# Optimization experiments

Measured on AMD Instinct MI355X. Metric: run time of the kernel, lower is better.

Reference implementation:

```python
import jax, jax.numpy as jnp
import numpy as np

TEMPERATURE = 12.5      # EMDLayer temperature
SINKHORN_EPS = 0.05     # entropic regularization for the batched EMD solve
SINKHORN_ITERS = 50     # fixed iteration count (jit-friendly)
WEIGHT_EPS = 1e-05      # OpenCVSolver adds 1e-5 after relu


def setup_inputs() -> dict:
    key = jax.random.key(0)
    k1, k2, k3 = jax.random.split(key, 3)
    E, Q, W, N = 4, 75, 5, 64
    similarity_map = jax.random.uniform(k1, (E, Q, W, N, N), dtype=jnp.float32)
    weight_1 = jax.random.uniform(k2, (E, Q, W, N), dtype=jnp.float32)
    weight_2 = jax.random.uniform(k3, (E, W, Q, N), dtype=jnp.float32)
    return {"similarity_map": similarity_map, "weight_1": weight_1, "weight_2": weight_2}


def _emd_flow(cost, a, b):
    """Batched entropic-regularized EMD (log-domain Sinkhorn).
    cost: [B, N, N]; a, b: [B, N] positive marginals (each sums to N).
    Returns flow: [B, N, N] with row sums ~a and col sums ~b."""
    logK = -cost / SINKHORN_EPS            # [B, N, N]
    log_a = jnp.log(a)
    log_b = jnp.log(b)

    def step(carry, _):
        log_u, log_v = carry
        log_u = log_a - jax.scipy.special.logsumexp(logK + log_v[:, None, :], axis=2)
        log_v = log_b - jax.scipy.special.logsumexp(logK + log_u[:, :, None], axis=1)
        return (log_u, log_v), None

    init = (jnp.zeros_like(log_a), jnp.zeros_like(log_b))
    (log_u, log_v), _ = jax.lax.scan(step, init, None, length=SINKHORN_ITERS)
    return jnp.exp(logK + log_u[:, :, None] + log_v[:, None, :])


def reference(similarity_map, weight_1, weight_2):
    E, Q, W, N, _ = similarity_map.shape
    sim = similarity_map.reshape(-1, N, N)                       # [B, N, N]
    w1 = weight_1.reshape(-1, N)                                  # [B, N]
    w2 = jnp.transpose(weight_2, (0, 2, 1, 3)).reshape(-1, N)     # transpose(1,2) then flatten

    # OpenCVSolver weight preprocessing: relu + eps, renormalize to sum N
    w1 = jax.nn.relu(w1) + WEIGHT_EPS
    w1 = w1 * (N / jnp.sum(w1, axis=1, keepdims=True))
    w2 = jax.nn.relu(w2) + WEIGHT_EPS
    w2 = w2 * (N / jnp.sum(w2, axis=1, keepdims=True))

    cost = 1.0 - sim
    flow = _emd_flow(cost, w1, w2)                                # [B, N, N]
    scores = jnp.sum(flow * sim, axis=(-1, -2)).reshape(E, Q, W)
    return scores * (TEMPERATURE / N)
```

## Files before the change

### kernel.cpp

```cpp
#include <hip/hip_runtime.h>

#define N 64
#define NPAD 65
#define ITERS 50
#define TEMP 12.5f
#define WEPS 1e-5f
#define QDIM 75
#define WDIM 5

__device__ __forceinline__ float waveReduceSum(float x) {
#pragma unroll
    for (int off = 32; off; off >>= 1) x += __shfl_xor(x, off, 64);
    return x;
}

__global__ __launch_bounds__(64) void emd_sinkhorn_kernel(
    const float* __restrict__ sim,
    const float* __restrict__ w1,
    const float* __restrict__ w2,
    float* __restrict__ out,
    int B)
{
    __shared__ __align__(16) float S[N * NPAD];
    __shared__ __align__(16) float U[N];
    __shared__ __align__(16) float V[N];

    const int b    = blockIdx.x;
    const int lane = threadIdx.x;
    const float* g = sim + (size_t)b * N * N;

    const float4* g4 = (const float4*)g;
#pragma unroll
    for (int t = 0; t < 16; ++t) {
        float4 x = g4[t * 64 + lane];
        int e0 = (t * 64 + lane) * 4;
        int r = e0 >> 6;
        int c = e0 & 63;
        S[r * NPAD + c + 0] = x.x;
        S[r * NPAD + c + 1] = x.y;
        S[r * NPAD + c + 2] = x.z;
        S[r * NPAD + c + 3] = x.w;
    }
    __syncthreads();

    float Krow[N], Kcol[N];
#pragma unroll
    for (int j = 0; j < N; ++j)
        Krow[j] = __expf((S[lane * NPAD + j] - 1.0f) * 20.0f);
#pragma unroll
    for (int i = 0; i < N; ++i)
        Kcol[i] = __expf((S[i * NPAD + lane] - 1.0f) * 20.0f);

    float a = w1[(size_t)b * N + lane];
    a = fmaxf(a, 0.0f) + WEPS;
    a *= (float)N / waveReduceSum(a);

    const int e   = b / (QDIM * WDIM);
    const int rem = b % (QDIM * WDIM);
    const int q   = rem / WDIM;
    const int w   = rem % WDIM;
    float bb = w2[((((size_t)e * WDIM + w) * QDIM) + q) * N + lane];
    bb = fmaxf(bb, 0.0f) + WEPS;
    bb *= (float)N / waveReduceSum(bb);

    V[lane] = 1.0f;
    __syncthreads();

    float u = 0.0f, v = 1.0f;
#pragma unroll 1
    for (int it = 0; it < ITERS; ++it) {
        const float4* V4 = (const float4*)V;
        float acc0 = 0, acc1 = 0, acc2 = 0, acc3 = 0;
#pragma unroll
        for (int j4 = 0; j4 < 16; ++j4) {
            float4 vv = V4[j4];
            acc0 = fmaf(Krow[4 * j4 + 0], vv.x, acc0);
            acc1 = fmaf(Krow[4 * j4 + 1], vv.y, acc1);
            acc2 = fmaf(Krow[4 * j4 + 2], vv.z, acc2);
            acc3 = fmaf(Krow[4 * j4 + 3], vv.w, acc3);
        }
        u = a * __builtin_amdgcn_rcpf((acc0 + acc1) + (acc2 + acc3));
        U[lane] = u;
        __syncthreads();

        const float4* U4 = (const float4*)U;
        acc0 = 0; acc1 = 0; acc2 = 0; acc3 = 0;
#pragma unroll
        for (int i4 = 0; i4 < 16; ++i4) {
            float4 uu = U4[i4];
            acc0 = fmaf(Kcol[4 * i4 + 0], uu.x, acc0);
            acc1 = fmaf(Kcol[4 * i4 + 1], uu.y, acc1);
            acc2 = fmaf(Kcol[4 * i4 + 2], uu.z, acc2);
            acc3 = fmaf(Kcol[4 * i4 + 3], uu.w, acc3);
        }
        v = bb * __builtin_amdgcn_rcpf((acc0 + acc1) + (acc2 + acc3));
        V[lane] = v;
        __syncthreads();
    }

    float s0 = 0, s1 = 0, s2 = 0, s3 = 0;
#pragma unroll
    for (int j4 = 0; j4 < 16; ++j4) {
        float4 vv = ((const float4*)V)[j4];
        s0 = fmaf(Krow[4 * j4 + 0] * S[lane * NPAD + 4 * j4 + 0], vv.x, s0);
        s1 = fmaf(Krow[4 * j4 + 1] * S[lane * NPAD + 4 * j4 + 1], vv.y, s1);
        s2 = fmaf(Krow[4 * j4 + 2] * S[lane * NPAD + 4 * j4 + 2], vv.z, s2);
        s3 = fmaf(Krow[4 * j4 + 3] * S[lane * NPAD + 4 * j4 + 3], vv.w, s3);
    }
    float partial = u * ((s0 + s1) + (s2 + s3));
    float tot = waveReduceSum(partial);
    if (lane == 0) out[b] = tot * (TEMP / (float)N);
}

extern "C" void kernel_launch(void* const* d_in, const int* in_sizes, int n_in,
                              void* d_out, int out_size, void* d_ws, size_t ws_size,
                              hipStream_t stream) {
    const float* sim = (const float*)d_in[0];
    const float* w1  = (const float*)d_in[1];
    const float* w2  = (const float*)d_in[2];
    float* out       = (float*)d_out;
    const int B = in_sizes[0] / (N * N);
    emd_sinkhorn_kernel<<<B, 64, 0, stream>>>(sim, w1, w2, out, B);
}
```

Measured before the change: 111.4 us.

## Split each Sinkhorn problem across four wavefronts with quad shuffle reductions

Each block now uses 256 threads instead of 64. Every row or column is handled by four lanes that each hold 16 kernel entries in registers and combine their partial dot products with xor shuffles. The per-thread register footprint drops from 128 kernel values to 32, and the serial dependent FMA chain per iteration gets shorter. In exchange, each half-iteration barrier now synchronises four wavefronts, and the redundant U/V shared-memory reads add LDS traffic.

```diff
diff --git a/kernel.cpp b/kernel.cpp
--- a/kernel.cpp
+++ b/kernel.cpp
@@ -14,102 +14,128 @@
     return x;
 }
 
-__global__ __launch_bounds__(64) void emd_sinkhorn_kernel(
+__global__ __launch_bounds__(256, 1) void emd_sinkhorn4w(
     const float* __restrict__ sim,
     const float* __restrict__ w1,
     const float* __restrict__ w2,
     float* __restrict__ out,
     int B)
 {
-    __shared__ __align__(16) float S[N * NPAD];
-    __shared__ __align__(16) float U[N];
-    __shared__ __align__(16) float V[N];
+    __shared__ float S[N * NPAD];
+    __shared__ __align__(16) float U[N], V[N], A[N], Bm[N];
+    __shared__ float Wred[4];
 
+    const int t    = threadIdx.x;
+    const int lane = t & 63;
+    const int wv   = t >> 6;
     const int b    = blockIdx.x;
-    const int lane = threadIdx.x;
-    const float* g = sim + (size_t)b * N * N;
+    const int r    = t >> 2;
+    const int j4   = t & 3;
+    const int c0   = j4 * 16;
 
-    const float4* g4 = (const float4*)g;
+    const float4* g4 = (const float4*)(sim + (size_t)b * N * N);
 #pragma unroll
-    for (int t = 0; t < 16; ++t) {
-        float4 x = g4[t * 64 + lane];
-        int e0 = (t * 64 + lane) * 4;
-        int r = e0 >> 6;
-        int c = e0 & 63;
-        S[r * NPAD + c + 0] = x.x;
-        S[r * NPAD + c + 1] = x.y;
-        S[r * NPAD + c + 2] = x.z;
-        S[r * NPAD + c + 3] = x.w;
+    for (int q = 0; q < 4; ++q) {
+        int idx = q * 256 + t;
+        float4 x = g4[idx];
+        int rr = idx >> 4;
+        int cc = (idx & 15) * 4;
+        S[rr * NPAD + cc + 0] = x.x;
+        S[rr * NPAD + cc + 1] = x.y;
+        S[rr * NPAD + cc + 2] = x.z;
+        S[rr * NPAD + cc + 3] = x.w;
+    }
+    if (wv == 0) {
+        float a = w1[(size_t)b * N + lane];
+        a = fmaxf(a, 0.0f) + WEPS;
+        a *= (float)N / waveReduceSum(a);
+        A[lane] = a;
+    } else if (wv == 1) {
+        const int e  = b / (QDIM * WDIM);
+        const int rm = b % (QDIM * WDIM);
+        const int q  = rm / WDIM, w = rm % WDIM;
+        float g = w2[((((size_t)e * WDIM + w) * QDIM) + q) * N + lane];
+        g = fmaxf(g, 0.0f) + WEPS;
+        g *= (float)N / waveReduceSum(g);
+        Bm[lane] = g;
+    } else if (wv == 2) {
+        V[lane] = 1.0f;
     }
     __syncthreads();
 
-    float Krow[N], Kcol[N];
+    float Kr[16], Kc[16];
 #pragma unroll
-    for (int j = 0; j < N; ++j)
-        Krow[j] = __expf((S[lane * NPAD + j] - 1.0f) * 20.0f);
-#pragma unroll
-    for (int i = 0; i < N; ++i)
-        Kcol[i] = __expf((S[i * NPAD + lane] - 1.0f) * 20.0f);
+    for (int k = 0; k < 16; ++k) {
+        Kr[k] = __expf((S[r * NPAD + c0 + k] - 1.0f) * 20.0f);
+        Kc[k] = __expf((S[(c0 + k) * NPAD + r] - 1.0f) * 20.0f);
+    }
+    const float a_reg = A[r];
+    const float b_reg = Bm[r];
 
-    float a = w1[(size_t)b * N + lane];
-    a = fmaxf(a, 0.0f) + WEPS;
-    a *= (float)N / waveReduceSum(a);
-
-    const int e   = b / (QDIM * WDIM);
-    const int rem = b % (QDIM * WDIM);
-    const int q   = rem / WDIM;
-    const int w   = rem % WDIM;
-    float bb = w2[((((size_t)e * WDIM + w) * QDIM) + q) * N + lane];
-    bb = fmaxf(bb, 0.0f) + WEPS;
-    bb *= (float)N / waveReduceSum(bb);
-
-    V[lane] = 1.0f;
-    __syncthreads();
-
-    float u = 0.0f, v = 1.0f;
+    float u = 0.0f;
 #pragma unroll 1
     for (int it = 0; it < ITERS; ++it) {
-        const float4* V4 = (const float4*)V;
-        float acc0 = 0, acc1 = 0, acc2 = 0, acc3 = 0;
-#pragma unroll
-        for (int j4 = 0; j4 < 16; ++j4) {
-            float4 vv = V4[j4];
-            acc0 = fmaf(Krow[4 * j4 + 0], vv.x, acc0);
-            acc1 = fmaf(Krow[4 * j4 + 1], vv.y, acc1);
-            acc2 = fmaf(Krow[4 * j4 + 2], vv.z, acc2);
-            acc3 = fmaf(Krow[4 * j4 + 3], vv.w, acc3);
+        {
+            const float4* V4 = (const float4*)(V + c0);
+            float4 x0 = V4[0], x1 = V4[1], x2 = V4[2], x3 = V4[3];
+            float p0 = 0, p1 = 0, p2 = 0, p3 = 0;
+            p0 = fmaf(Kr[ 0], x0.x, p0); p1 = fmaf(Kr[ 1], x0.y, p1);
+            p2 = fmaf(Kr[ 2], x0.z, p2); p3 = fmaf(Kr[ 3], x0.w, p3);
+            p0 = fmaf(Kr[ 4], x1.x, p0); p1 = fmaf(Kr[ 5], x1.y, p1);
+            p2 = fmaf(Kr[ 6], x1.z, p2); p3 = fmaf(Kr[ 7], x1.w, p3);
+            p0 = fmaf(Kr[ 8], x2.x, p0); p1 = fmaf(Kr[ 9], x2.y, p1);
+            p2 = fmaf(Kr[10], x2.z, p2); p3 = fmaf(Kr[11], x2.w, p3);
+            p0 = fmaf(Kr[12], x3.x, p0); p1 = fmaf(Kr[13], x3.y, p1);
+            p2 = fmaf(Kr[14], x3.z, p2); p3 = fmaf(Kr[15], x3.w, p3);
+            float s = (p0 + p1) + (p2 + p3);
+            s += __shfl_xor(s, 1, 64);
+            s += __shfl_xor(s, 2, 64);
+            u = a_reg * __builtin_amdgcn_rcpf(s);
+            if (j4 == 0) U[r] = u;
         }
-        u = a * __builtin_amdgcn_rcpf((acc0 + acc1) + (acc2 + acc3));
-        U[lane] = u;
         __syncthreads();
 
-        const float4* U4 = (const float4*)U;
-        acc0 = 0; acc1 = 0; acc2 = 0; acc3 = 0;
-#pragma unroll
-        for (int i4 = 0; i4 < 16; ++i4) {
-            float4 uu = U4[i4];
-            acc0 = fmaf(Kcol[4 * i4 + 0], uu.x, acc0);
-            acc1 = fmaf(Kcol[4 * i4 + 1], uu.y, acc1);
-            acc2 = fmaf(Kcol[4 * i4 + 2], uu.z, acc2);
-            acc3 = fmaf(Kcol[4 * i4 + 3], uu.w, acc3);
+        {
+            const float4* U4 = (const float4*)(U + c0);
+            float4 x0 = U4[0], x1 = U4[1], x2 = U4[2], x3 = U4[3];
+            float p0 = 0, p1 = 0, p2 = 0, p3 = 0;
+            p0 = fmaf(Kc[ 0], x0.x, p0); p1 = fmaf(Kc[ 1], x0.y, p1);
+            p2 = fmaf(Kc[ 2], x0.z, p2); p3 = fmaf(Kc[ 3], x0.w, p3);
+            p0 = fmaf(Kc[ 4], x1.x, p0); p1 = fmaf(Kc[ 5], x1.y, p1);
+            p2 = fmaf(Kc[ 6], x1.z, p2); p3 = fmaf(Kc[ 7], x1.w, p3);
+            p0 = fmaf(Kc[ 8], x2.x, p0); p1 = fmaf(Kc[ 9], x2.y, p1);
+            p2 = fmaf(Kc[10], x2.z, p2); p3 = fmaf(Kc[11], x2.w, p3);
+            p0 = fmaf(Kc[12], x3.x, p0); p1 = fmaf(Kc[13], x3.y, p1);
+            p2 = fmaf(Kc[14], x3.z, p2); p3 = fmaf(Kc[15], x3.w, p3);
+            float s = (p0 + p1) + (p2 + p3);
+            s += __shfl_xor(s, 1, 64);
+            s += __shfl_xor(s, 2, 64);
+            float v = b_reg * __builtin_amdgcn_rcpf(s);
+            if (j4 == 0) V[r] = v;
         }
-        v = bb * __builtin_amdgcn_rcpf((acc0 + acc1) + (acc2 + acc3));
-        V[lane] = v;
         __syncthreads();
     }
 
-    float s0 = 0, s1 = 0, s2 = 0, s3 = 0;
-#pragma unroll
-    for (int j4 = 0; j4 < 16; ++j4) {
-        float4 vv = ((const float4*)V)[j4];
-        s0 = fmaf(Krow[4 * j4 + 0] * S[lane * NPAD + 4 * j4 + 0], vv.x, s0);
-        s1 = fmaf(Krow[4 * j4 + 1] * S[lane * NPAD + 4 * j4 + 1], vv.y, s1);
-        s2 = fmaf(Krow[4 * j4 + 2] * S[lane * NPAD + 4 * j4 + 2], vv.z, s2);
-        s3 = fmaf(Krow[4 * j4 + 3] * S[lane * NPAD + 4 * j4 + 3], vv.w, s3);
+    {
+        const float4* V4 = (const float4*)(V + c0);
+        float4 x0 = V4[0], x1 = V4[1], x2 = V4[2], x3 = V4[3];
+        float p0 = 0, p1 = 0, p2 = 0, p3 = 0;
+        const float* Srow = S + r * NPAD + c0;
+        p0 = fmaf(Kr[ 0] * Srow[ 0], x0.x, p0); p1 = fmaf(Kr[ 1] * Srow[ 1], x0.y, p1);
+        p2 = fmaf(Kr[ 2] * Srow[ 2], x0.z, p2); p3 = fmaf(Kr[ 3] * Srow[ 3], x0.w, p3);
+        p0 = fmaf(Kr[ 4] * Srow[ 4], x1.x, p0); p1 = fmaf(Kr[ 5] * Srow[ 5], x1.y, p1);
+        p2 = fmaf(Kr[ 6] * Srow[ 6], x1.z, p2); p3 = fmaf(Kr[ 7] * Srow[ 7], x1.w, p3);
+        p0 = fmaf(Kr[ 8] * Srow[ 8], x2.x, p0); p1 = fmaf(Kr[ 9] * Srow[ 9], x2.y, p1);
+        p2 = fmaf(Kr[10] * Srow[10], x2.z, p2); p3 = fmaf(Kr[11] * Srow[11], x2.w, p3);
+        p0 = fmaf(Kr[12] * Srow[12], x3.x, p0); p1 = fmaf(Kr[13] * Srow[13], x3.y, p1);
+        p2 = fmaf(Kr[14] * Srow[14], x3.z, p2); p3 = fmaf(Kr[15] * Srow[15], x3.w, p3);
+        float part = u * ((p0 + p1) + (p2 + p3));
+        float ws = waveReduceSum(part);
+        if (lane == 0) Wred[wv] = ws;
     }
-    float partial = u * ((s0 + s1) + (s2 + s3));
-    float tot = waveReduceSum(partial);
-    if (lane == 0) out[b] = tot * (TEMP / (float)N);
+    __syncthreads();
+    if (t == 0)
+        out[b] = (Wred[0] + Wred[1] + Wred[2] + Wred[3]) * (TEMP / (float)N);
 }
 
 extern "C" void kernel_launch(void* const* d_in, const int* in_sizes, int n_in,
@@ -120,5 +146,5 @@
     const float* w2  = (const float*)d_in[2];
     float* out       = (float*)d_out;
     const int B = in_sizes[0] / (N * N);
-    emd_sinkhorn_kernel<<<B, 64, 0, stream>>>(sim, w1, w2, out, B);
+    emd_sinkhorn4w<<<B, 256, 0, stream>>>(sim, w1, w2, out, B);
 }
```

Result: slower. 113.7 us (+2.1%).

## Tile Sinkhorn matvecs as 4x16 register blocks with DPP quad reductions

Applied to the files above, without the earlier changes.

Each lane now holds a 4-row by 16-column block of the kernel matrix for both the row and column passes. Partial sums are combined across the quad with DPP xor shuffles, which replaces each lane reading all 64 entries of U/V from LDS. This cuts LDS broadcast reads per iteration and drops the 16KB shared staging of the similarity tile, since K is loaded directly from global memory. The final score recovers sim from K through log2 instead of keeping S in shared memory, which adds transcendental work and a small precision risk.

```diff
diff --git a/kernel.cpp b/kernel.cpp
--- a/kernel.cpp
+++ b/kernel.cpp
@@ -1,12 +1,14 @@
 #include <hip/hip_runtime.h>
 
 #define N 64
-#define NPAD 65
 #define ITERS 50
 #define TEMP 12.5f
 #define WEPS 1e-5f
 #define QDIM 75
 #define WDIM 5
+
+#define DPP_XOR1(x) __int_as_float(__builtin_amdgcn_update_dpp(0, __float_as_int(x), 0xB1, 0xF, 0xF, true))
+#define DPP_XOR2(x) __int_as_float(__builtin_amdgcn_update_dpp(0, __float_as_int(x), 0x4E, 0xF, 0xF, true))
 
 __device__ __forceinline__ float waveReduceSum(float x) {
 #pragma unroll
@@ -14,102 +16,138 @@
     return x;
 }
 
-__global__ __launch_bounds__(64) void emd_sinkhorn_kernel(
+__global__ __launch_bounds__(64, 1) void emd_tile(
     const float* __restrict__ sim,
     const float* __restrict__ w1,
     const float* __restrict__ w2,
     float* __restrict__ out,
     int B)
 {
-    __shared__ __align__(16) float S[N * NPAD];
-    __shared__ __align__(16) float U[N];
-    __shared__ __align__(16) float V[N];
+    __shared__ __align__(16) float S[128];
 
+    const int lane = threadIdx.x;
     const int b    = blockIdx.x;
-    const int lane = threadIdx.x;
-    const float* g = sim + (size_t)b * N * N;
+    const int g    = lane >> 2;
+    const int s    = lane & 3;
+    const float* gm = sim + (size_t)b * N * N;
 
-    const float4* g4 = (const float4*)g;
+    float Kr[4][16], Kc[4][16];
 #pragma unroll
-    for (int t = 0; t < 16; ++t) {
-        float4 x = g4[t * 64 + lane];
-        int e0 = (t * 64 + lane) * 4;
-        int r = e0 >> 6;
-        int c = e0 & 63;
-        S[r * NPAD + c + 0] = x.x;
-        S[r * NPAD + c + 1] = x.y;
-        S[r * NPAD + c + 2] = x.z;
-        S[r * NPAD + c + 3] = x.w;
+    for (int k = 0; k < 4; ++k)
+#pragma unroll
+        for (int m = 0; m < 4; ++m) {
+            float4 x = *(const float4*)(gm + (4 * g + k) * N + 16 * s + 4 * m);
+            Kr[k][4 * m + 0] = __expf((x.x - 1.0f) * 20.0f);
+            Kr[k][4 * m + 1] = __expf((x.y - 1.0f) * 20.0f);
+            Kr[k][4 * m + 2] = __expf((x.z - 1.0f) * 20.0f);
+            Kr[k][4 * m + 3] = __expf((x.w - 1.0f) * 20.0f);
+        }
+#pragma unroll
+    for (int j = 0; j < 16; ++j) {
+        float4 x = *(const float4*)(gm + (16 * s + j) * N + 4 * g);
+        Kc[0][j] = __expf((x.x - 1.0f) * 20.0f);
+        Kc[1][j] = __expf((x.y - 1.0f) * 20.0f);
+        Kc[2][j] = __expf((x.z - 1.0f) * 20.0f);
+        Kc[3][j] = __expf((x.w - 1.0f) * 20.0f);
     }
+#pragma unroll
+    for (int k = 0; k < 4; ++k)
+#pragma unroll
+        for (int j = 0; j < 16; ++j) {
+            asm volatile("" : "+v"(Kr[k][j]));
+            asm volatile("" : "+v"(Kc[k][j]));
+        }
+
+    float a_own = w1[(size_t)b * N + lane];
+    a_own = fmaxf(a_own, 0.0f) + WEPS;
+    a_own *= (float)N / waveReduceSum(a_own);
+
+    const int e  = b / (QDIM * WDIM);
+    const int rm = b % (QDIM * WDIM);
+    const int q  = rm / WDIM, w = rm % WDIM;
+    float b_own = w2[((((size_t)e * WDIM + w) * QDIM) + q) * N + lane];
+    b_own = fmaxf(b_own, 0.0f) + WEPS;
+    b_own *= (float)N / waveReduceSum(b_own);
+
+    S[64 + lane] = 1.0f;
     __syncthreads();
 
-    float Krow[N], Kcol[N];
-#pragma unroll
-    for (int j = 0; j < N; ++j)
-        Krow[j] = __expf((S[lane * NPAD + j] - 1.0f) * 20.0f);
-#pragma unroll
-    for (int i = 0; i < N; ++i)
-        Kcol[i] = __expf((S[i * NPAD + lane] - 1.0f) * 20.0f);
-
-    float a = w1[(size_t)b * N + lane];
-    a = fmaxf(a, 0.0f) + WEPS;
-    a *= (float)N / waveReduceSum(a);
-
-    const int e   = b / (QDIM * WDIM);
-    const int rem = b % (QDIM * WDIM);
-    const int q   = rem / WDIM;
-    const int w   = rem % WDIM;
-    float bb = w2[((((size_t)e * WDIM + w) * QDIM) + q) * N + lane];
-    bb = fmaxf(bb, 0.0f) + WEPS;
-    bb *= (float)N / waveReduceSum(bb);
-
-    V[lane] = 1.0f;
-    __syncthreads();
-
-    float u = 0.0f, v = 1.0f;
 #pragma unroll 1
     for (int it = 0; it < ITERS; ++it) {
-        const float4* V4 = (const float4*)V;
-        float acc0 = 0, acc1 = 0, acc2 = 0, acc3 = 0;
-#pragma unroll
-        for (int j4 = 0; j4 < 16; ++j4) {
-            float4 vv = V4[j4];
-            acc0 = fmaf(Krow[4 * j4 + 0], vv.x, acc0);
-            acc1 = fmaf(Krow[4 * j4 + 1], vv.y, acc1);
-            acc2 = fmaf(Krow[4 * j4 + 2], vv.z, acc2);
-            acc3 = fmaf(Krow[4 * j4 + 3], vv.w, acc3);
+        {
+            const float4* V4 = (const float4*)&S[64 + 16 * s];
+            float4 x0 = V4[0], x1 = V4[1], x2 = V4[2], x3 = V4[3];
+            float acc0 = 0, acc1 = 0, acc2 = 0, acc3 = 0;
+#define ROWF(k, acc)                                                        \
+            acc = fmaf(Kr[k][ 0], x0.x, acc); acc = fmaf(Kr[k][ 1], x0.y, acc); \
+            acc = fmaf(Kr[k][ 2], x0.z, acc); acc = fmaf(Kr[k][ 3], x0.w, acc); \
+            acc = fmaf(Kr[k][ 4], x1.x, acc); acc = fmaf(Kr[k][ 5], x1.y, acc); \
+            acc = fmaf(Kr[k][ 6], x1.z, acc); acc = fmaf(Kr[k][ 7], x1.w, acc); \
+            acc = fmaf(Kr[k][ 8], x2.x, acc); acc = fmaf(Kr[k][ 9], x2.y, acc); \
+            acc = fmaf(Kr[k][10], x2.z, acc); acc = fmaf(Kr[k][11], x2.w, acc); \
+            acc = fmaf(Kr[k][12], x3.x, acc); acc = fmaf(Kr[k][13], x3.y, acc); \
+            acc = fmaf(Kr[k][14], x3.z, acc); acc = fmaf(Kr[k][15], x3.w, acc)
+            ROWF(0, acc0); ROWF(1, acc1); ROWF(2, acc2); ROWF(3, acc3);
+            acc0 += DPP_XOR1(acc0); acc1 += DPP_XOR1(acc1);
+            acc2 += DPP_XOR1(acc2); acc3 += DPP_XOR1(acc3);
+            acc0 += DPP_XOR2(acc0); acc1 += DPP_XOR2(acc1);
+            acc2 += DPP_XOR2(acc2); acc3 += DPP_XOR2(acc3);
+            float ab = (s & 1) ? acc1 : acc0;
+            float cd = (s & 1) ? acc3 : acc2;
+            float se = (s & 2) ? cd : ab;
+            S[lane] = a_own * __builtin_amdgcn_rcpf(se);
         }
-        u = a * __builtin_amdgcn_rcpf((acc0 + acc1) + (acc2 + acc3));
-        U[lane] = u;
         __syncthreads();
 
-        const float4* U4 = (const float4*)U;
-        acc0 = 0; acc1 = 0; acc2 = 0; acc3 = 0;
-#pragma unroll
-        for (int i4 = 0; i4 < 16; ++i4) {
-            float4 uu = U4[i4];
-            acc0 = fmaf(Kcol[4 * i4 + 0], uu.x, acc0);
-            acc1 = fmaf(Kcol[4 * i4 + 1], uu.y, acc1);
-            acc2 = fmaf(Kcol[4 * i4 + 2], uu.z, acc2);
-            acc3 = fmaf(Kcol[4 * i4 + 3], uu.w, acc3);
+        {
+            const float4* U4 = (const float4*)&S[16 * s];
+            float4 x0 = U4[0], x1 = U4[1], x2 = U4[2], x3 = U4[3];
+            float acc0 = 0, acc1 = 0, acc2 = 0, acc3 = 0;
+#define COLF(k, acc)                                                        \
+            acc = fmaf(Kc[k][ 0], x0.x, acc); acc = fmaf(Kc[k][ 1], x0.y, acc); \
+            acc = fmaf(Kc[k][ 2], x0.z, acc); acc = fmaf(Kc[k][ 3], x0.w, acc); \
+            acc = fmaf(Kc[k][ 4], x1.x, acc); acc = fmaf(Kc[k][ 5], x1.y, acc); \
+            acc = fmaf(Kc[k][ 6], x1.z, acc); acc = fmaf(Kc[k][ 7], x1.w, acc); \
+            acc = fmaf(Kc[k][ 8], x2.x, acc); acc = fmaf(Kc[k][ 9], x2.y, acc); \
+            acc = fmaf(Kc[k][10], x2.z, acc); acc = fmaf(Kc[k][11], x2.w, acc); \
+            acc = fmaf(Kc[k][12], x3.x, acc); acc = fmaf(Kc[k][13], x3.y, acc); \
+            acc = fmaf(Kc[k][14], x3.z, acc); acc = fmaf(Kc[k][15], x3.w, acc)
+            COLF(0, acc0); COLF(1, acc1); COLF(2, acc2); COLF(3, acc3);
+            acc0 += DPP_XOR1(acc0); acc1 += DPP_XOR1(acc1);
+            acc2 += DPP_XOR1(acc2); acc3 += DPP_XOR1(acc3);
+            acc0 += DPP_XOR2(acc0); acc1 += DPP_XOR2(acc1);
+            acc2 += DPP_XOR2(acc2); acc3 += DPP_XOR2(acc3);
+            float ab = (s & 1) ? acc1 : acc0;
+            float cd = (s & 1) ? acc3 : acc2;
+            float se = (s & 2) ? cd : ab;
+            S[64 + lane] = b_own * __builtin_amdgcn_rcpf(se);
         }
-        v = bb * __builtin_amdgcn_rcpf((acc0 + acc1) + (acc2 + acc3));
-        V[lane] = v;
         __syncthreads();
     }
 
-    float s0 = 0, s1 = 0, s2 = 0, s3 = 0;
+    {
+        float4 u4 = *(const float4*)&S[4 * g];
+        const float4* V4 = (const float4*)&S[64 + 16 * s];
+        float4 x0 = V4[0], x1 = V4[1], x2 = V4[2], x3 = V4[3];
+        float vj[16] = {x0.x, x0.y, x0.z, x0.w, x1.x, x1.y, x1.z, x1.w,
+                        x2.x, x2.y, x2.z, x2.w, x3.x, x3.y, x3.z, x3.w};
+        float uk[4] = {u4.x, u4.y, u4.z, u4.w};
+        const float c = 0.69314718056f / 20.0f;
+        float p = 0.0f;
 #pragma unroll
-    for (int j4 = 0; j4 < 16; ++j4) {
-        float4 vv = ((const float4*)V)[j4];
-        s0 = fmaf(Krow[4 * j4 + 0] * S[lane * NPAD + 4 * j4 + 0], vv.x, s0);
-        s1 = fmaf(Krow[4 * j4 + 1] * S[lane * NPAD + 4 * j4 + 1], vv.y, s1);
-        s2 = fmaf(Krow[4 * j4 + 2] * S[lane * NPAD + 4 * j4 + 2], vv.z, s2);
-        s3 = fmaf(Krow[4 * j4 + 3] * S[lane * NPAD + 4 * j4 + 3], vv.w, s3);
+        for (int k = 0; k < 4; ++k) {
+            float rs = 0.0f;
+#pragma unroll
+            for (int j = 0; j < 16; ++j) {
+                float kk = Kr[k][j];
+                float sv = fmaf(__log2f(kk), c, 1.0f);
+                rs = fmaf(kk * sv, vj[j], rs);
+            }
+            p = fmaf(uk[k], rs, p);
+        }
+        float tot = waveReduceSum(p);
+        if (lane == 0) out[b] = tot * (TEMP / (float)N);
     }
-    float partial = u * ((s0 + s1) + (s2 + s3));
-    float tot = waveReduceSum(partial);
-    if (lane == 0) out[b] = tot * (TEMP / (float)N);
 }
 
 extern "C" void kernel_launch(void* const* d_in, const int* in_sizes, int n_in,
@@ -120,5 +158,5 @@
     const float* w2  = (const float*)d_in[2];
     float* out       = (float*)d_out;
     const int B = in_sizes[0] / (N * N);
-    emd_sinkhorn_kernel<<<B, 64, 0, stream>>>(sim, w1, w2, out, B);
+    emd_tile<<<B, 64, 0, stream>>>(sim, w1, w2, out, B);
 }
```

New measurement: 101.8 us. 1.09x faster.
